# Kernel tuning notes

Hardware: AMD Instinct MI355X
Metric: run time of the kernel (lower is better)

Reference implementation:

```python
import jax, jax.numpy as jnp
import numpy as np

NUM_EMBEDDINGS = 1024
EMBEDDING_DIM = 256


def setup_inputs() -> dict:
    key = jax.random.key(0)
    k_in, k_w = jax.random.split(key)
    inputs = jax.random.normal(k_in, (32, EMBEDDING_DIM, 2048), dtype=jnp.float32)
    # nn.Embedding weight initialized uniform in [-1/K, 1/K]
    bound = 1.0 / NUM_EMBEDDINGS
    weight = jax.random.uniform(k_w, (NUM_EMBEDDINGS, EMBEDDING_DIM),
                                dtype=jnp.float32, minval=-bound, maxval=bound)
    return {"inputs": inputs, "weight": weight}


def reference(inputs, weight):
    B, D, T = inputs.shape
    # [B, D, T] -> [B*T, D]
    flat = jnp.transpose(inputs, (0, 2, 1)).reshape(-1, D)
    distances = (jnp.sum(flat * flat, axis=1, keepdims=True)
                 + jnp.sum(weight * weight, axis=1)
                 - 2.0 * flat @ weight.T)  # [N, K]
    encoding_indices = jnp.argmin(distances, axis=1)  # [N]
    # one-hot @ weight is just a gather
    quantized = weight[encoding_indices].reshape(B, T, D)  # [B, T, D]
    quantized = jnp.transpose(quantized, (0, 2, 1))  # [B, D, T]
    # straight-through estimator
    quantized = inputs + jax.lax.stop_gradient(quantized - inputs)
    return quantized, encoding_indices[:, None]
```

## Files before the change

kernel.cpp:

```cpp
#include <hip/hip_runtime.h>


#define VQ_B   32
#define VQ_D   256
#define VQ_T   2048
#define VQ_K   1024

typedef _Float16 f16x8 __attribute__((ext_vector_type(8)));
typedef _Float16 f16x4 __attribute__((ext_vector_type(4)));
typedef float    f32x4 __attribute__((ext_vector_type(4)));

#define GLOAD_LDS16(gaddr, laddr) \
  __builtin_amdgcn_global_load_lds((const __attribute__((address_space(1))) void*)(gaddr), \
                                   (__attribute__((address_space(3))) void*)(laddr), 16, 0, 0)

__global__ __launch_bounds__(256) void vq_prep_kernel(
    const float* __restrict__ inp, const float* __restrict__ w,
    _Float16* __restrict__ Xh, _Float16* __restrict__ Xl,
    float* __restrict__ xnorm,
    float* __restrict__ wnorm,
    _Float16* __restrict__ Wh, _Float16* __restrict__ Wl)
{
    __shared__ double sbuf[256];
    const int tid = threadIdx.x;
    if (blockIdx.x < 512) {
        const int t    = tid & 127;
        const int half = tid >> 7;
        const int b    = blockIdx.x >> 4;
        const int tg   = (blockIdx.x & 15) * 128 + t;
        const float* p = inp + (size_t)b * VQ_D * VQ_T + tg;

        double s = 0.0;
        #pragma unroll 4
        for (int dc = half * 16; dc < half * 16 + 16; ++dc) {
            float x[8];
            #pragma unroll
            for (int j = 0; j < 8; ++j)
                x[j] = p[(size_t)(dc * 8 + j) * VQ_T];
            f16x8 hv, lv;
            #pragma unroll
            for (int j = 0; j < 8; ++j) {
                s += (double)x[j] * (double)x[j];
                const _Float16 h = (_Float16)x[j];
                hv[j] = h;
                lv[j] = (_Float16)((x[j] - (float)h) * 16777216.0f);
            }
            const size_t off = (((size_t)b * 32 + dc) * VQ_T + tg) * 8;
            *(f16x8*)(Xh + off) = hv;
            *(f16x8*)(Xl + off) = lv;
        }
        if (half) sbuf[t] = s;
        __syncthreads();
        if (!half) xnorm[(size_t)b * VQ_T + tg] = (float)(s + sbuf[t]);
    } else {
        double (*ws_)[16] = (double(*)[16])sbuf;
        const int kk = tid >> 4;
        const int dg = tid & 15;
        const int k  = (blockIdx.x - 512) * 16 + kk;
        const float* src = w + (size_t)k * VQ_D + dg * 16;
        double s = 0.0;
        #pragma unroll
        for (int q = 0; q < 4; ++q) {
            float4 v = *(const float4*)(src + q * 4);
            s += (double)v.x * v.x + (double)v.y * v.y
               + (double)v.z * v.z + (double)v.w * v.w;
            const float e4[4] = {v.x, v.y, v.z, v.w};
            f16x4 hv, lv;
            #pragma unroll
            for (int j = 0; j < 4; ++j) {
                const float es = e4[j] * 1024.0f;
                const _Float16 h = (_Float16)es;
                hv[j] = h;
                lv[j] = (_Float16)((es - (float)h) * 16777216.0f);
            }
            *(f16x4*)(Wh + (size_t)k * VQ_D + dg * 16 + q * 4) = hv;
            *(f16x4*)(Wl + (size_t)k * VQ_D + dg * 16 + q * 4) = lv;
        }
        ws_[kk][dg] = s;
        __syncthreads();
        if (dg == 0) {
            double acc = 0.0;
            #pragma unroll
            for (int g = 0; g < 16; ++g) acc += ws_[kk][g];
            wnorm[k] = (float)acc;
        }
    }
}

__global__ __launch_bounds__(256, 2) void vq_mfma_kernel(
    const _Float16* __restrict__ Wh, const _Float16* __restrict__ Wl,
    const _Float16* __restrict__ Xh, const _Float16* __restrict__ Xl,
    const float* __restrict__ wnorm, const float* __restrict__ xnorm,
    const float* __restrict__ w,
    float* __restrict__ outq, float* __restrict__ outi)
{
    __shared__ alignas(16) char stg[2][32768];
    const int tid  = threadIdx.x;
    const int lane = tid & 63;
    const int wv   = tid >> 6;
    const int m16  = lane & 15;
    const int quad = lane >> 4;
    const int wm   = wv & 1;
    const int wn   = wv >> 1;
    const int b    = blockIdx.x >> 4;
    const int tt0  = (blockIdx.x & 15) * 128;
    const long bt  = (long)b * VQ_T + tt0;

    float xnr[4];
    #pragma unroll
    for (int fn = 0; fn < 4; ++fn)
        xnr[fn] = xnorm[bt + wn * 64 + fn * 16 + m16];

    const char* gp[8];
    #pragma unroll
    for (int i = 0; i < 8; ++i) {
        const int hf = i >> 2, f = i & 3;
        if (wv < 2) {
            const char* baseW = (const char*)((wv & 1) ? Wl : Wh);
            gp[i] = baseW + (size_t)(hf * 64 + f * 16 + m16) * 512 + quad * 16;
        } else {
            const char* baseX = (const char*)((wv & 1) ? Xl : Xh);
            gp[i] = baseX + (((size_t)b * 32 + quad) * 2048
                             + (tt0 + hf * 64 + f * 16 + m16)) * 16;
        }
    }
    auto advance = [&](int q) {
        if ((q & 7) == 7) {
            #pragma unroll
            for (int i = 0; i < 8; ++i)
                gp[i] += (wv < 2) ? (long)(65536 - 448) : (long)(-7) * 131072;
        } else {
            #pragma unroll
            for (int i = 0; i < 8; ++i)
                gp[i] += (wv < 2) ? 64L : 131072L;
        }
    };

    float bestv[4] = {3.0e38f, 3.0e38f, 3.0e38f, 3.0e38f};
    int   besti[4] = {0, 0, 0, 0};
    f32x4 acch[4][4], accl[4][4];

    #pragma unroll
    for (int i = 0; i < 8; ++i)
        GLOAD_LDS16(gp[i], &stg[0][(wv * 8 + i) * 1024]);
    advance(0);

    for (int s = 0; s < 64; ++s) {
        const int cur = s & 1;
        if ((s & 7) == 0) {
            #pragma unroll
            for (int fm = 0; fm < 4; ++fm)
                #pragma unroll
                for (int fn = 0; fn < 4; ++fn) {
                    acch[fm][fn] = (f32x4){0.f, 0.f, 0.f, 0.f};
                    accl[fm][fn] = (f32x4){0.f, 0.f, 0.f, 0.f};
                }
        }
        __syncthreads();
        if (s < 63) {
            #pragma unroll
            for (int i = 0; i < 8; ++i)
                GLOAD_LDS16(gp[i], &stg[cur ^ 1][(wv * 8 + i) * 1024]);
            advance(s + 1);
        }

        const char* base = stg[cur];
        f16x8 ah[4], al[4], bh[4], bl[4];
        #pragma unroll
        for (int f = 0; f < 4; ++f) {
            ah[f] = *(const f16x8*)(base + ((wm * 4 + f)) * 1024 + lane * 16);
            al[f] = *(const f16x8*)(base + ((8 + wm * 4 + f)) * 1024 + lane * 16);
            bh[f] = *(const f16x8*)(base + ((16 + wn * 4 + f)) * 1024 + lane * 16);
            bl[f] = *(const f16x8*)(base + ((24 + wn * 4 + f)) * 1024 + lane * 16);
        }
        #pragma unroll
        for (int fm = 0; fm < 4; ++fm)
            #pragma unroll
            for (int fn = 0; fn < 4; ++fn) {
                acch[fm][fn] = __builtin_amdgcn_mfma_f32_16x16x32_f16(
                    ah[fm], bh[fn], acch[fm][fn], 0, 0, 0);
                accl[fm][fn] = __builtin_amdgcn_mfma_f32_16x16x32_f16(
                    ah[fm], bl[fn], accl[fm][fn], 0, 0, 0);
                accl[fm][fn] = __builtin_amdgcn_mfma_f32_16x16x32_f16(
                    al[fm], bh[fn], accl[fm][fn], 0, 0, 0);
            }

        if ((s & 7) == 7) {
            const int k0 = (s >> 3) * 128;
            #pragma unroll
            for (int fm = 0; fm < 4; ++fm) {
                #pragma unroll
                for (int r = 0; r < 4; ++r) {
                    const int kg = k0 + wm * 64 + fm * 16 + quad * 4 + r;
                    const float wnk = wnorm[kg];
                    #pragma unroll
                    for (int fn = 0; fn < 4; ++fn) {
                        const float t1 = xnr[fn] + wnk;
                        const float d2 = (acch[fm][fn][r]
                                          + accl[fm][fn][r] * 5.9604644775390625e-8f)
                                         * 0.001953125f;
                        const float sc = t1 - d2;
                        if (sc < bestv[fn]) { bestv[fn] = sc; besti[fn] = kg; }
                    }
                }
            }
        }
    }

    float rv[4]; int ri[4];
    #pragma unroll
    for (int fn = 0; fn < 4; ++fn) {
        float bv = bestv[fn]; int bi = besti[fn];
        #pragma unroll
        for (int mask = 16; mask <= 32; mask <<= 1) {
            const float ov = __shfl_xor(bv, mask, 64);
            const int   oi = __shfl_xor(bi, mask, 64);
            if (ov < bv || (ov == bv && oi < bi)) { bv = ov; bi = oi; }
        }
        rv[fn] = bv; ri[fn] = bi;
    }

    __syncthreads();
    float* sv = (float*)stg[0];
    int*   si = (int*)(stg[0] + 1024);
    if (quad == 0) {
        #pragma unroll
        for (int fn = 0; fn < 4; ++fn) {
            const int tl = wn * 64 + fn * 16 + m16;
            sv[wm * 128 + tl] = rv[fn];
            si[wm * 128 + tl] = ri[fn];
        }
    }
    __syncthreads();
    if (tid < 128) {
        const float v0 = sv[tid], v1 = sv[128 + tid];
        const int   i0 = si[tid], i1 = si[128 + tid];
        const int   bi = (v1 < v0 || (v1 == v0 && i1 < i0)) ? i1 : i0;
        si[tid] = bi;
        outi[bt + tid] = (float)bi;
    }
    __syncthreads();

    {
        const int t  = tid & 127;
        const int dh = tid >> 7;
        const int bi = si[t];
        const float* wrow = w + (size_t)bi * VQ_D + dh * 128;
        float* obase = outq + ((size_t)b * VQ_D + (size_t)dh * 128) * VQ_T + tt0 + t;
        #pragma unroll 4
        for (int dd = 0; dd < 128; dd += 4) {
            float4 v = *(const float4*)(wrow + dd);
            obase[(size_t)(dd + 0) * VQ_T] = v.x;
            obase[(size_t)(dd + 1) * VQ_T] = v.y;
            obase[(size_t)(dd + 2) * VQ_T] = v.z;
            obase[(size_t)(dd + 3) * VQ_T] = v.w;
        }
    }
}

extern "C" void kernel_launch(void* const* d_in, const int* in_sizes, int n_in,
                              void* d_out, int out_size, void* d_ws, size_t ws_size,
                              hipStream_t stream) {
    const float* inp = (const float*)d_in[0];
    const float* w   = (const float*)d_in[1];
    float* outq  = (float*)d_out;
    float* outi  = outq + (size_t)VQ_B * VQ_D * VQ_T;

    float*    wnorm = (float*)d_ws;
    float*    xnorm = wnorm + VQ_K;
    _Float16* Wh    = (_Float16*)(xnorm + VQ_B * VQ_T);
    _Float16* Wl    = Wh + (size_t)VQ_K * VQ_D;
    _Float16* Xh    = Wl + (size_t)VQ_K * VQ_D;
    _Float16* Xl    = Xh + (size_t)VQ_B * VQ_T * VQ_D;

    vq_prep_kernel<<<dim3(512 + VQ_K / 16), dim3(256), 0, stream>>>(
        inp, w, Xh, Xl, xnorm, wnorm, Wh, Wl);
    vq_mfma_kernel<<<dim3(VQ_B * (VQ_T / 128)), dim3(256), 0, stream>>>(
        Wh, Wl, Xh, Xl, wnorm, xnorm, w, outq, outi);
}
```

Before: 241.7 us.

## Fuse input fp16 split and norm into MFMA kernel, drop X prep pass

The prep kernel no longer converts the input into separate fp16 high/low buffers or computes x norms. The main kernel instead streams fp32 input tiles directly into LDS through a swizzled layout and builds the fp16 high/low MFMA operands in registers. It also accumulates the x squared norms during the first eight steps and shares them through LDS. This removes a full write and re-read of the split input buffers and a kernel launch. In exchange, every K-chunk pass repeats the conversion ALU work and uses scalar LDS reads, which may cost bank conflicts.

```diff
diff --git a/kernel.cpp b/kernel.cpp
--- a/kernel.cpp
+++ b/kernel.cpp
@@ -14,87 +14,53 @@
   __builtin_amdgcn_global_load_lds((const __attribute__((address_space(1))) void*)(gaddr), \
                                    (__attribute__((address_space(3))) void*)(laddr), 16, 0, 0)
 
-__global__ __launch_bounds__(256) void vq_prep_kernel(
-    const float* __restrict__ inp, const float* __restrict__ w,
-    _Float16* __restrict__ Xh, _Float16* __restrict__ Xl,
-    float* __restrict__ xnorm,
-    float* __restrict__ wnorm,
+__global__ __launch_bounds__(256) void vq_wprep_kernel(
+    const float* __restrict__ w, float* __restrict__ wnorm,
     _Float16* __restrict__ Wh, _Float16* __restrict__ Wl)
 {
-    __shared__ double sbuf[256];
+    __shared__ double ws_[16][16];
     const int tid = threadIdx.x;
-    if (blockIdx.x < 512) {
-        const int t    = tid & 127;
-        const int half = tid >> 7;
-        const int b    = blockIdx.x >> 4;
-        const int tg   = (blockIdx.x & 15) * 128 + t;
-        const float* p = inp + (size_t)b * VQ_D * VQ_T + tg;
-
-        double s = 0.0;
-        #pragma unroll 4
-        for (int dc = half * 16; dc < half * 16 + 16; ++dc) {
-            float x[8];
-            #pragma unroll
-            for (int j = 0; j < 8; ++j)
-                x[j] = p[(size_t)(dc * 8 + j) * VQ_T];
-            f16x8 hv, lv;
-            #pragma unroll
-            for (int j = 0; j < 8; ++j) {
-                s += (double)x[j] * (double)x[j];
-                const _Float16 h = (_Float16)x[j];
-                hv[j] = h;
-                lv[j] = (_Float16)((x[j] - (float)h) * 16777216.0f);
-            }
-            const size_t off = (((size_t)b * 32 + dc) * VQ_T + tg) * 8;
-            *(f16x8*)(Xh + off) = hv;
-            *(f16x8*)(Xl + off) = lv;
-        }
-        if (half) sbuf[t] = s;
-        __syncthreads();
-        if (!half) xnorm[(size_t)b * VQ_T + tg] = (float)(s + sbuf[t]);
-    } else {
-        double (*ws_)[16] = (double(*)[16])sbuf;
-        const int kk = tid >> 4;
-        const int dg = tid & 15;
-        const int k  = (blockIdx.x - 512) * 16 + kk;
-        const float* src = w + (size_t)k * VQ_D + dg * 16;
-        double s = 0.0;
-        #pragma unroll
-        for (int q = 0; q < 4; ++q) {
-            float4 v = *(const float4*)(src + q * 4);
-            s += (double)v.x * v.x + (double)v.y * v.y
-               + (double)v.z * v.z + (double)v.w * v.w;
-            const float e4[4] = {v.x, v.y, v.z, v.w};
-            f16x4 hv, lv;
-            #pragma unroll
-            for (int j = 0; j < 4; ++j) {
-                const float es = e4[j] * 1024.0f;
-                const _Float16 h = (_Float16)es;
-                hv[j] = h;
-                lv[j] = (_Float16)((es - (float)h) * 16777216.0f);
-            }
-            *(f16x4*)(Wh + (size_t)k * VQ_D + dg * 16 + q * 4) = hv;
-            *(f16x4*)(Wl + (size_t)k * VQ_D + dg * 16 + q * 4) = lv;
-        }
-        ws_[kk][dg] = s;
-        __syncthreads();
-        if (dg == 0) {
-            double acc = 0.0;
-            #pragma unroll
-            for (int g = 0; g < 16; ++g) acc += ws_[kk][g];
-            wnorm[k] = (float)acc;
-        }
+    const int kk  = tid >> 4;
+    const int dg  = tid & 15;
+    const int k   = blockIdx.x * 16 + kk;
+    const float* src = w + (size_t)k * VQ_D + dg * 16;
+    double s = 0.0;
+    #pragma unroll
+    for (int q = 0; q < 4; ++q) {
+        float4 v = *(const float4*)(src + q * 4);
+        s += (double)v.x * v.x + (double)v.y * v.y
+           + (double)v.z * v.z + (double)v.w * v.w;
+        const float e4[4] = {v.x, v.y, v.z, v.w};
+        f16x4 hv, lv;
+        #pragma unroll
+        for (int j = 0; j < 4; ++j) {
+            const float es = e4[j] * 1024.0f;
+            const _Float16 h = (_Float16)es;
+            hv[j] = h;
+            lv[j] = (_Float16)((es - (float)h) * 16777216.0f);
+        }
+        *(f16x4*)(Wh + (size_t)k * VQ_D + dg * 16 + q * 4) = hv;
+        *(f16x4*)(Wl + (size_t)k * VQ_D + dg * 16 + q * 4) = lv;
+    }
+    ws_[kk][dg] = s;
+    __syncthreads();
+    if (dg == 0) {
+        double acc = 0.0;
+        #pragma unroll
+        for (int g = 0; g < 16; ++g) acc += ws_[kk][g];
+        wnorm[k] = (float)acc;
     }
 }
 
 __global__ __launch_bounds__(256, 2) void vq_mfma_kernel(
     const _Float16* __restrict__ Wh, const _Float16* __restrict__ Wl,
-    const _Float16* __restrict__ Xh, const _Float16* __restrict__ Xl,
-    const float* __restrict__ wnorm, const float* __restrict__ xnorm,
+    const float* __restrict__ inp,
+    const float* __restrict__ wnorm,
     const float* __restrict__ w,
     float* __restrict__ outq, float* __restrict__ outi)
 {
     __shared__ alignas(16) char stg[2][32768];
+    __shared__ double xs[2][128];
     const int tid  = threadIdx.x;
     const int lane = tid & 63;
     const int wv   = tid >> 6;
@@ -106,35 +72,45 @@
     const int tt0  = (blockIdx.x & 15) * 128;
     const long bt  = (long)b * VQ_T + tt0;
 
-    float xnr[4];
-    #pragma unroll
-    for (int fn = 0; fn < 4; ++fn)
-        xnr[fn] = xnorm[bt + wn * 64 + fn * 16 + m16];
-
     const char* gp[8];
     #pragma unroll
     for (int i = 0; i < 8; ++i) {
-        const int hf = i >> 2, f = i & 3;
         if (wv < 2) {
+            const int hf = i >> 2, f = i & 3;
             const char* baseW = (const char*)((wv & 1) ? Wl : Wh);
             gp[i] = baseW + (size_t)(hf * 64 + f * 16 + m16) * 512 + quad * 16;
         } else {
-            const char* baseX = (const char*)((wv & 1) ? Xl : Xh);
-            gp[i] = baseX + (((size_t)b * 32 + quad) * 2048
-                             + (tt0 + hf * 64 + f * 16 + m16)) * 16;
+            const int r  = (wv - 2) * 16 + i * 2 + (lane >> 5);
+            const int sw = ((wv - 2) * 2 + (i >> 2)) * 2;
+            gp[i] = (const char*)inp
+                  + ((size_t)b * VQ_D + r) * (size_t)(VQ_T * 4)
+                  + (size_t)(tt0 * 4)
+                  + (size_t)(((lane & 31) ^ sw) * 16);
         }
     }
     auto advance = [&](int q) {
         if ((q & 7) == 7) {
             #pragma unroll
             for (int i = 0; i < 8; ++i)
-                gp[i] += (wv < 2) ? (long)(65536 - 448) : (long)(-7) * 131072;
+                gp[i] += (wv < 2) ? (long)(65536 - 448) : (long)(-7) * 262144;
         } else {
             #pragma unroll
             for (int i = 0; i < 8; ++i)
-                gp[i] += (wv < 2) ? 64L : 131072L;
+                gp[i] += (wv < 2) ? 64L : 262144L;
         }
     };
+
+    int tsw[4];
+    #pragma unroll
+    for (int f = 0; f < 4; ++f) {
+        const int tl = wn * 64 + f * 16 + m16;
+        tsw[f] = (((tl >> 2) ^ (quad * 2)) << 2) | (tl & 3);
+    }
+
+    const int xt_t  = tid & 127;
+    const int xhalf = tid >> 7;
+    double xacc = 0.0;
+    float  xnr[4];
 
     float bestv[4] = {3.0e38f, 3.0e38f, 3.0e38f, 3.0e38f};
     int   besti[4] = {0, 0, 0, 0};
@@ -164,15 +140,28 @@
             advance(s + 1);
         }
 
-        const char* base = stg[cur];
+        const char*  base  = stg[cur];
+        const float* xtile = (const float*)(base + 16384);
+
         f16x8 ah[4], al[4], bh[4], bl[4];
         #pragma unroll
         for (int f = 0; f < 4; ++f) {
             ah[f] = *(const f16x8*)(base + ((wm * 4 + f)) * 1024 + lane * 16);
             al[f] = *(const f16x8*)(base + ((8 + wm * 4 + f)) * 1024 + lane * 16);
-            bh[f] = *(const f16x8*)(base + ((16 + wn * 4 + f)) * 1024 + lane * 16);
-            bl[f] = *(const f16x8*)(base + ((24 + wn * 4 + f)) * 1024 + lane * 16);
-        }
+        }
+        #pragma unroll
+        for (int f = 0; f < 4; ++f) {
+            f16x8 hv, lv;
+            #pragma unroll
+            for (int j = 0; j < 8; ++j) {
+                const float x = xtile[(quad * 8 + j) * 128 + tsw[f]];
+                const _Float16 h = (_Float16)x;
+                hv[j] = h;
+                lv[j] = (_Float16)((x - (float)h) * 16777216.0f);
+            }
+            bh[f] = hv; bl[f] = lv;
+        }
+
         #pragma unroll
         for (int fm = 0; fm < 4; ++fm)
             #pragma unroll
@@ -184,6 +173,24 @@
                 accl[fm][fn] = __builtin_amdgcn_mfma_f32_16x16x32_f16(
                     al[fm], bh[fn], accl[fm][fn], 0, 0, 0);
             }
+
+        if (s < 8 && (s >> 2) == xhalf) {
+            #pragma unroll
+            for (int dd = 0; dd < 32; ++dd) {
+                const float x = xtile[dd * 128 +
+                    ((((xt_t >> 2) ^ ((dd >> 3) * 2)) << 2) | (xt_t & 3))];
+                xacc += (double)x * (double)x;
+            }
+        }
+        if (s == 7) {
+            xs[xhalf][xt_t] = xacc;
+            __syncthreads();
+            #pragma unroll
+            for (int fn = 0; fn < 4; ++fn) {
+                const int tl = wn * 64 + fn * 16 + m16;
+                xnr[fn] = (float)(xs[0][tl] + xs[1][tl]);
+            }
+        }
 
         if ((s & 7) == 7) {
             const int k0 = (s >> 3) * 128;
@@ -267,14 +274,10 @@
     float* outi  = outq + (size_t)VQ_B * VQ_D * VQ_T;
 
     float*    wnorm = (float*)d_ws;
-    float*    xnorm = wnorm + VQ_K;
-    _Float16* Wh    = (_Float16*)(xnorm + VQ_B * VQ_T);
+    _Float16* Wh    = (_Float16*)(wnorm + VQ_K);
     _Float16* Wl    = Wh + (size_t)VQ_K * VQ_D;
-    _Float16* Xh    = Wl + (size_t)VQ_K * VQ_D;
-    _Float16* Xl    = Xh + (size_t)VQ_B * VQ_T * VQ_D;
-
-    vq_prep_kernel<<<dim3(512 + VQ_K / 16), dim3(256), 0, stream>>>(
-        inp, w, Xh, Xl, xnorm, wnorm, Wh, Wl);
+
+    vq_wprep_kernel<<<dim3(VQ_K / 16), dim3(256), 0, stream>>>(w, wnorm, Wh, Wl);
     vq_mfma_kernel<<<dim3(VQ_B * (VQ_T / 128)), dim3(256), 0, stream>>>(
-        Wh, Wl, Xh, Xl, wnorm, xnorm, w, outq, outi);
+        Wh, Wl, inp, wnorm, w, outq, outi);
 }
```

New measurement: 251.8 us. 1.04x slower.

## Fuse input fp16 split and norm computation into the MFMA kernel prologue

Applied to the files above, without the earlier changes.

Input conversion to fp16 hi/lo and the x-norm computation move out of the prep kernel into the start of each MFMA block, which handles its own 128-token tile. Each thread now reads float4 along T and covers four tokens. The prep kernel is left handling only the codebook. This cuts the prep launch's share of the work, but the Xh/Xl tiles are still written to global memory and read back by the same block. That round trip depends on visibility of global writes after a block barrier, and the block carries the conversion latency before its MFMA loop starts.

```diff
diff --git a/kernel.cpp b/kernel.cpp
--- a/kernel.cpp
+++ b/kernel.cpp
@@ -14,83 +14,49 @@
   __builtin_amdgcn_global_load_lds((const __attribute__((address_space(1))) void*)(gaddr), \
                                    (__attribute__((address_space(3))) void*)(laddr), 16, 0, 0)
 
-__global__ __launch_bounds__(256) void vq_prep_kernel(
-    const float* __restrict__ inp, const float* __restrict__ w,
-    _Float16* __restrict__ Xh, _Float16* __restrict__ Xl,
-    float* __restrict__ xnorm,
-    float* __restrict__ wnorm,
+__global__ __launch_bounds__(256) void vq_wprep_kernel(
+    const float* __restrict__ w, float* __restrict__ wnorm,
     _Float16* __restrict__ Wh, _Float16* __restrict__ Wl)
 {
-    __shared__ double sbuf[256];
+    __shared__ double ws_[16][16];
     const int tid = threadIdx.x;
-    if (blockIdx.x < 512) {
-        const int t    = tid & 127;
-        const int half = tid >> 7;
-        const int b    = blockIdx.x >> 4;
-        const int tg   = (blockIdx.x & 15) * 128 + t;
-        const float* p = inp + (size_t)b * VQ_D * VQ_T + tg;
-
-        double s = 0.0;
-        #pragma unroll 4
-        for (int dc = half * 16; dc < half * 16 + 16; ++dc) {
-            float x[8];
-            #pragma unroll
-            for (int j = 0; j < 8; ++j)
-                x[j] = p[(size_t)(dc * 8 + j) * VQ_T];
-            f16x8 hv, lv;
-            #pragma unroll
-            for (int j = 0; j < 8; ++j) {
-                s += (double)x[j] * (double)x[j];
-                const _Float16 h = (_Float16)x[j];
-                hv[j] = h;
-                lv[j] = (_Float16)((x[j] - (float)h) * 16777216.0f);
-            }
-            const size_t off = (((size_t)b * 32 + dc) * VQ_T + tg) * 8;
-            *(f16x8*)(Xh + off) = hv;
-            *(f16x8*)(Xl + off) = lv;
-        }
-        if (half) sbuf[t] = s;
-        __syncthreads();
-        if (!half) xnorm[(size_t)b * VQ_T + tg] = (float)(s + sbuf[t]);
-    } else {
-        double (*ws_)[16] = (double(*)[16])sbuf;
-        const int kk = tid >> 4;
-        const int dg = tid & 15;
-        const int k  = (blockIdx.x - 512) * 16 + kk;
-        const float* src = w + (size_t)k * VQ_D + dg * 16;
-        double s = 0.0;
-        #pragma unroll
-        for (int q = 0; q < 4; ++q) {
-            float4 v = *(const float4*)(src + q * 4);
-            s += (double)v.x * v.x + (double)v.y * v.y
-               + (double)v.z * v.z + (double)v.w * v.w;
-            const float e4[4] = {v.x, v.y, v.z, v.w};
-            f16x4 hv, lv;
-            #pragma unroll
-            for (int j = 0; j < 4; ++j) {
-                const float es = e4[j] * 1024.0f;
-                const _Float16 h = (_Float16)es;
-                hv[j] = h;
-                lv[j] = (_Float16)((es - (float)h) * 16777216.0f);
-            }
-            *(f16x4*)(Wh + (size_t)k * VQ_D + dg * 16 + q * 4) = hv;
-            *(f16x4*)(Wl + (size_t)k * VQ_D + dg * 16 + q * 4) = lv;
-        }
-        ws_[kk][dg] = s;
-        __syncthreads();
-        if (dg == 0) {
-            double acc = 0.0;
-            #pragma unroll
-            for (int g = 0; g < 16; ++g) acc += ws_[kk][g];
-            wnorm[k] = (float)acc;
-        }
+    const int kk  = tid >> 4;
+    const int dg  = tid & 15;
+    const int k   = blockIdx.x * 16 + kk;
+    const float* src = w + (size_t)k * VQ_D + dg * 16;
+    double s = 0.0;
+    #pragma unroll
+    for (int q = 0; q < 4; ++q) {
+        float4 v = *(const float4*)(src + q * 4);
+        s += (double)v.x * v.x + (double)v.y * v.y
+           + (double)v.z * v.z + (double)v.w * v.w;
+        const float e4[4] = {v.x, v.y, v.z, v.w};
+        f16x4 hv, lv;
+        #pragma unroll
+        for (int j = 0; j < 4; ++j) {
+            const float es = e4[j] * 1024.0f;
+            const _Float16 h = (_Float16)es;
+            hv[j] = h;
+            lv[j] = (_Float16)((es - (float)h) * 16777216.0f);
+        }
+        *(f16x4*)(Wh + (size_t)k * VQ_D + dg * 16 + q * 4) = hv;
+        *(f16x4*)(Wl + (size_t)k * VQ_D + dg * 16 + q * 4) = lv;
+    }
+    ws_[kk][dg] = s;
+    __syncthreads();
+    if (dg == 0) {
+        double acc = 0.0;
+        #pragma unroll
+        for (int g = 0; g < 16; ++g) acc += ws_[kk][g];
+        wnorm[k] = (float)acc;
     }
 }
 
 __global__ __launch_bounds__(256, 2) void vq_mfma_kernel(
     const _Float16* __restrict__ Wh, const _Float16* __restrict__ Wl,
-    const _Float16* __restrict__ Xh, const _Float16* __restrict__ Xl,
-    const float* __restrict__ wnorm, const float* __restrict__ xnorm,
+    const float* __restrict__ inp,
+    _Float16* __restrict__ Xh, _Float16* __restrict__ Xl,
+    float* __restrict__ wnorm, float* __restrict__ xnorm,
     const float* __restrict__ w,
     float* __restrict__ outq, float* __restrict__ outi)
 {
@@ -105,6 +71,48 @@
     const int b    = blockIdx.x >> 4;
     const int tt0  = (blockIdx.x & 15) * 128;
     const long bt  = (long)b * VQ_T + tt0;
+
+    {
+        double* xpart = (double*)stg;
+        const int t4 = (tid & 31) * 4;
+        const int ds = tid >> 5;
+        const float* p = inp + (size_t)b * VQ_D * VQ_T + tt0 + t4;
+        double s4[4] = {0.0, 0.0, 0.0, 0.0};
+        #pragma unroll
+        for (int dc = ds * 4; dc < ds * 4 + 4; ++dc) {
+            f16x8 hvv[4], lvv[4];
+            #pragma unroll
+            for (int j = 0; j < 8; ++j) {
+                const float4 v = *(const float4*)(p + (size_t)(dc * 8 + j) * VQ_T);
+                const float xx[4] = {v.x, v.y, v.z, v.w};
+                #pragma unroll
+                for (int tt = 0; tt < 4; ++tt) {
+                    const float x = xx[tt];
+                    s4[tt] += (double)x * (double)x;
+                    const _Float16 h = (_Float16)x;
+                    hvv[tt][j] = h;
+                    lvv[tt][j] = (_Float16)((x - (float)h) * 16777216.0f);
+                }
+            }
+            #pragma unroll
+            for (int tt = 0; tt < 4; ++tt) {
+                const size_t off = (((size_t)b * 32 + dc) * VQ_T + tt0 + t4 + tt) * 8;
+                *(f16x8*)(Xh + off) = hvv[tt];
+                *(f16x8*)(Xl + off) = lvv[tt];
+            }
+        }
+        #pragma unroll
+        for (int tt = 0; tt < 4; ++tt)
+            xpart[ds * 128 + t4 + tt] = s4[tt];
+        __syncthreads();
+        if (tid < 128) {
+            double s = xpart[tid];
+            #pragma unroll
+            for (int sl = 1; sl < 8; ++sl) s += xpart[sl * 128 + tid];
+            xnorm[(size_t)b * VQ_T + tt0 + tid] = (float)s;
+        }
+        __syncthreads();
+    }
 
     float xnr[4];
     #pragma unroll
@@ -273,8 +281,7 @@
     _Float16* Xh    = Wl + (size_t)VQ_K * VQ_D;
     _Float16* Xl    = Xh + (size_t)VQ_B * VQ_T * VQ_D;
 
-    vq_prep_kernel<<<dim3(512 + VQ_K / 16), dim3(256), 0, stream>>>(
-        inp, w, Xh, Xl, xnorm, wnorm, Wh, Wl);
+    vq_wprep_kernel<<<dim3(VQ_K / 16), dim3(256), 0, stream>>>(w, wnorm, Wh, Wl);
     vq_mfma_kernel<<<dim3(VQ_B * (VQ_T / 128)), dim3(256), 0, stream>>>(
-        Wh, Wl, Xh, Xl, wnorm, xnorm, w, outq, outi);
+        Wh, Wl, inp, Xh, Xl, wnorm, xnorm, w, outq, outi);
 }
```

Result: slower. 247.1 us (+2.2%).
